# Optimization experiments

Measured on AMD Instinct MI355X. Metric: run time of the kernel, lower is better.

The kernel has to match this reference:

```python
import jax, jax.numpy as jnp
import numpy as np

B, T, D, H, E, O = 4, 2048, 512, 2048, 4, 512
C = 1024  # expert capacity
HE = H // E  # per-expert hidden width


def setup_inputs() -> dict:
    key = jax.random.key(0)
    ks = jax.random.split(key, 7)
    x = jax.random.normal(ks[0], (B, T, D), dtype=jnp.float32)
    dispatch_mask = jax.random.uniform(ks[1], (B, T, E, C), dtype=jnp.float32)
    combine_array = jax.random.uniform(ks[2], (B, T, E, C), dtype=jnp.float32)
    # per-expert parameters (fc1 contract, fc2 expand)
    w1 = jax.random.normal(ks[3], (E, D, HE), dtype=jnp.float32) * (1.0 / np.sqrt(D))
    b1 = jnp.zeros((E, HE), dtype=jnp.float32)
    w2 = jax.random.normal(ks[4], (E, HE, O), dtype=jnp.float32) * (1.0 / np.sqrt(HE))
    b2 = jnp.zeros((O,), dtype=jnp.float32)
    return {"x": x, "dispatch_mask": dispatch_mask, "combine_array": combine_array,
            "w1": w1, "b1": b1, "w2": w2, "b2": b2}


def reference(x, dispatch_mask, combine_array, w1, b1, w2, b2):
    # dispatch: gather tokens into per-expert capacity buffers [B,E,C,D]
    xd = jnp.einsum('btd,btec->becd', x, dispatch_mask)
    # per-expert fc1: [B,E,C,HE]
    h = jnp.einsum('becd,edh->bech', xd, w1) + b1[None, :, None, :]
    # GELU (exact erf form, matching torch nn.GELU default); norm/dropout are identity
    h = jax.nn.gelu(h, approximate=False)
    # per-expert fc2: [B,E,C,O]
    y = jnp.einsum('bech,eho->beco', h, w2)
    # combine: scatter expert outputs back to tokens [B,T,O]
    out = jnp.einsum('beco,btec->bto', y, combine_array) + b2
    return out
```

## Files before the change

### kernel.cpp

```cpp
#include <hip/hip_runtime.h>
#include <math.h>

namespace {

typedef short short8 __attribute__((ext_vector_type(8)));
typedef float f32x4 __attribute__((ext_vector_type(4)));

constexpr int kB = 4, kT = 2048, kD = 512, kE = 4, kC = 1024, kHE = 512,
              kO = 512, kEC = 4096;

__device__ __forceinline__ unsigned short f2bf(float f) {
    unsigned int u = __float_as_uint(f);
    u += 0x7fffu + ((u >> 16) & 1u);
    return (unsigned short)(u >> 16);
}

__device__ __forceinline__ float gelu_exact(float v) {
    return 0.5f * v * (1.0f + erff(v * 0.70710678118654752f));
}

#define GLDS16(g, l)                                                      \
    __builtin_amdgcn_global_load_lds(                                     \
        (const __attribute__((address_space(1))) unsigned int*)(g),       \
        (__attribute__((address_space(3))) unsigned int*)(l), 16, 0, 0)

__global__ __launch_bounds__(256)
void transpose_cast(const float* __restrict__ in, unsigned short* __restrict__ out,
                    int R, int Cc, long long sIn, long long sOut)
{
    __shared__ float tile[32][33];
    const int z = blockIdx.z;
    const float* ip = in + (long long)z * sIn;
    unsigned short* op = out + (long long)z * sOut;
    const int c0 = blockIdx.x * 32, r0 = blockIdx.y * 32;
    const int tx = threadIdx.x & 31, ty = threadIdx.x >> 5;
#pragma unroll
    for (int i = 0; i < 4; ++i) {
        const int r = ty + i * 8;
        tile[r][tx] = ip[(size_t)(r0 + r) * Cc + c0 + tx];
    }
    __syncthreads();
#pragma unroll
    for (int i = 0; i < 4; ++i) {
        const int c = ty + i * 8;
        op[(size_t)(c0 + c) * R + r0 + tx] = f2bf(tile[tx][c]);
    }
}

__global__ __launch_bounds__(256)
void cast_bf16(const float* __restrict__ in, unsigned short* __restrict__ out,
               long long n)
{
    const long long i = ((long long)blockIdx.x * blockDim.x + threadIdx.x) * 4;
    if (i < n) {
        const float4 v = *(const float4*)&in[i];
        unsigned short o[4] = {f2bf(v.x), f2bf(v.y), f2bf(v.z), f2bf(v.w)};
        *(uint2*)&out[i] = *(const uint2*)o;
    }
}

template <int MODE>
__global__ __launch_bounds__(256, 2)
void mfma_gemm(const unsigned short* __restrict__ Aall,
               const unsigned short* __restrict__ Ball,
               const float* __restrict__ biasAll,
               void* __restrict__ Call,
               int M, int N, int K,
               long long sA, long long sB, long long sC,
               int zModA, int zModB, int zModBias, int biasStride, int bShift)
{
    __shared__ unsigned short As[2][128 * 64];
    __shared__ unsigned short Bs[2][128 * 64];

    const int z = blockIdx.z;
    const unsigned short* Ab = Aall + (long long)(z % zModA) * sA;
    const unsigned short* Bb = Ball + (long long)(z % zModB) * sB;
    const float* bias =
        (MODE != 0) ? biasAll + (long long)(z % zModBias) * biasStride : nullptr;

    const int t = threadIdx.x;
    const int lane = t & 63;
    const int w = t >> 6;
    const int wrow = w * 32;
    const int l8r = lane >> 3;
    const int l8c = ((lane & 7) ^ l8r) * 8;
    const int row0 = blockIdx.y * 128;
    const int col0 = blockIdx.x * 128;

    const int wm = (w >> 1) * 64;
    const int wn = (w & 1) * 64;
    const int fr = lane & 15;
    const int fq = (lane >> 4) * 8;
    const int fsw = (fr & 7) * 8;

    const unsigned int bMask = (1u << bShift) - 1u;

    f32x4 acc[4][4] = {};

#define STAGE(buf, k0)                                                        \
    do {                                                                      \
        _Pragma("unroll")                                                     \
        for (int r = 0; r < 4; ++r) {                                         \
            const int ar = row0 + wrow + r * 8 + l8r;                         \
            GLDS16(Ab + (size_t)ar * K + ((k0) + l8c),                        \
                   &As[buf][(wrow + r * 8) * 64]);                            \
            const int bn = col0 + wrow + r * 8 + l8r;                         \
            const int gk = (k0) + l8c;                                        \
            const size_t boff =                                               \
                (((size_t)(gk >> bShift) * N + bn) << bShift) + (gk & bMask); \
            GLDS16(Bb + boff, &Bs[buf][(wrow + r * 8) * 64]);                 \
        }                                                                     \
    } while (0)

    const int nt = K / 64;
    STAGE(0, 0);
    int cur = 0;
    for (int t0 = 0; t0 < nt; ++t0) {
        if (t0 + 1 < nt) {
            STAGE(cur ^ 1, (t0 + 1) * 64);
            asm volatile("s_waitcnt vmcnt(8)" ::: "memory");
        } else {
            asm volatile("s_waitcnt vmcnt(0)" ::: "memory");
        }
        __builtin_amdgcn_s_barrier();
#pragma unroll
        for (int kk = 0; kk < 2; ++kk) {
            short8 af[4], bf[4];
#pragma unroll
            for (int i = 0; i < 4; ++i)
                af[i] = *(const short8*)&As[cur][(wm + i * 16 + fr) * 64 +
                                                 ((kk * 32 + fq) ^ fsw)];
#pragma unroll
            for (int j = 0; j < 4; ++j)
                bf[j] = *(const short8*)&Bs[cur][(wn + j * 16 + fr) * 64 +
                                                 ((kk * 32 + fq) ^ fsw)];
#pragma unroll
            for (int i = 0; i < 4; ++i)
#pragma unroll
                for (int j = 0; j < 4; ++j)
                    acc[i][j] = __builtin_amdgcn_mfma_f32_16x16x32_bf16(
                        af[i], bf[j], acc[i][j], 0, 0, 0);
        }
        asm volatile("s_waitcnt lgkmcnt(0)" ::: "memory");
        __builtin_amdgcn_sched_barrier(0);
        __builtin_amdgcn_s_barrier();
        cur ^= 1;
    }
#undef STAGE

    const long long cz = (long long)z * sC;
#pragma unroll
    for (int i = 0; i < 4; ++i) {
        const int rowb = row0 + wm + i * 16 + (lane >> 4) * 4;
#pragma unroll
        for (int j = 0; j < 4; ++j) {
            const int col = col0 + wn + j * 16 + fr;
            const float bv = (MODE != 0) ? bias[col] : 0.0f;
#pragma unroll
            for (int r = 0; r < 4; ++r) {
                const float v = acc[i][j][r];
                const size_t idx = (size_t)cz + (size_t)(rowb + r) * N + col;
                if (MODE == 0)
                    ((unsigned short*)Call)[idx] = f2bf(v);
                else if (MODE == 1)
                    ((unsigned short*)Call)[idx] = f2bf(gelu_exact(v + bv));
                else
                    ((float*)Call)[idx] = v + bv;
            }
        }
    }
}

}

extern "C" void kernel_launch(void* const* d_in, const int* in_sizes, int n_in,
                              void* d_out, int out_size, void* d_ws, size_t ws_size,
                              hipStream_t stream)
{
    const float* x    = (const float*)d_in[0];
    const float* mask = (const float*)d_in[1];
    const float* comb = (const float*)d_in[2];
    const float* w1   = (const float*)d_in[3];
    const float* b1   = (const float*)d_in[4];
    const float* w2   = (const float*)d_in[5];
    const float* b2   = (const float*)d_in[6];
    float* out = (float*)d_out;

    unsigned short* ws    = (unsigned short*)d_ws;
    unsigned short* regA  = ws;
    unsigned short* xT    = regA + 33554432;
    unsigned short* w1T   = xT + 4194304;
    unsigned short* w2T   = w1T + 1048576;
    unsigned short* xd    = w2T + 1048576;
    unsigned short* h     = xd + 8388608;
    unsigned short* maskT = regA;
    unsigned short* combB = regA;
    unsigned short* yT    = xd;

    dim3 blk(256);

    transpose_cast<<<dim3(kEC / 32, kT / 32, kB), blk, 0, stream>>>(
        mask, maskT, kT, kEC, (long long)kT * kEC, (long long)kT * kEC);
    transpose_cast<<<dim3(kD / 32, kT / 32, kB), blk, 0, stream>>>(
        x, xT, kT, kD, (long long)kT * kD, (long long)kT * kD);
    transpose_cast<<<dim3(kHE / 32, kD / 32, kE), blk, 0, stream>>>(
        w1, w1T, kD, kHE, (long long)kD * kHE, (long long)kD * kHE);
    transpose_cast<<<dim3(kO / 32, kHE / 32, kE), blk, 0, stream>>>(
        w2, w2T, kHE, kO, (long long)kHE * kO, (long long)kHE * kO);

    mfma_gemm<0><<<dim3(kD / 128, kEC / 128, kB), blk, 0, stream>>>(
        maskT, xT, nullptr, xd, kEC, kD, kT,
        (long long)kEC * kT, (long long)kD * kT, (long long)kEC * kD,
        kB, kB, 1, 0, 11);

    cast_bf16<<<dim3(33554432 / 4 / 256), blk, 0, stream>>>(
        comb, combB, 33554432LL);

    mfma_gemm<1><<<dim3(kHE / 128, kC / 128, kB * kE), blk, 0, stream>>>(
        xd, w1T, b1, h, kC, kHE, kD,
        (long long)kC * kD, (long long)kHE * kD, (long long)kC * kHE,
        kB * kE, kE, kE, kHE, 9);

    mfma_gemm<0><<<dim3(kC / 128, kO / 128, kB * kE), blk, 0, stream>>>(
        w2T, h, nullptr, yT, kO, kC, kHE,
        (long long)kO * kHE, (long long)kC * kHE, (long long)kO * kC,
        kE, kB * kE, 1, 0, 9);

    mfma_gemm<3><<<dim3(kO / 128, kT / 128, kB), blk, 0, stream>>>(
        combB, yT, b2, out, kT, kO, kEC,
        (long long)kT * kEC, (long long)kE * kO * kC, (long long)kT * kO,
        kB, kB, 1, 0, 10);
}
```

Measured before the change: 477.2 us.

## Deepen GEMM pipeline to 4 LDS stages with register double-buffered fragments

Changes the bf16 MFMA GEMM from a 2-stage LDS double buffer to a 4-stage ring. LDS fragment reads for the next k-tile are issued with inline ds_read_b128 asm into a second register set while the current set feeds the MFMAs, which removes one barrier per iteration. It also remaps workgroup IDs in groups of 8, likely to improve L2 locality across dies. The cost is double the LDS and more registers, so launch bounds drop to one block per CU-slot and occupancy falls. The loop assumes K/64 is at least 4 and that gridDim.x is a power of two.

New measurement: 442.9 us. 7.2% less time.

```diff
diff --git a/kernel.cpp b/kernel.cpp
--- a/kernel.cpp
+++ b/kernel.cpp
@@ -4,6 +4,7 @@
 namespace {
 
 typedef short short8 __attribute__((ext_vector_type(8)));
+typedef int i32x4 __attribute__((ext_vector_type(4)));
 typedef float f32x4 __attribute__((ext_vector_type(4)));
 
 constexpr int kB = 4, kT = 2048, kD = 512, kE = 4, kC = 1024, kHE = 512,
@@ -60,7 +61,7 @@
 }
 
 template <int MODE>
-__global__ __launch_bounds__(256, 2)
+__global__ __launch_bounds__(256, 1)
 void mfma_gemm(const unsigned short* __restrict__ Aall,
                const unsigned short* __restrict__ Ball,
                const float* __restrict__ biasAll,
@@ -69,14 +70,27 @@
                long long sA, long long sB, long long sC,
                int zModA, int zModB, int zModBias, int biasStride, int bShift)
 {
-    __shared__ unsigned short As[2][128 * 64];
-    __shared__ unsigned short Bs[2][128 * 64];
+    __shared__ unsigned short As[4][128 * 64];
+    __shared__ unsigned short Bs[4][128 * 64];
 
     const int z = blockIdx.z;
     const unsigned short* Ab = Aall + (long long)(z % zModA) * sA;
     const unsigned short* Bb = Ball + (long long)(z % zModB) * sB;
     const float* bias =
         (MODE != 0) ? biasAll + (long long)(z % zModBias) * biasStride : nullptr;
+
+    const int gx = gridDim.x;
+    int lin = blockIdx.y * gx + blockIdx.x;
+    const int nwg = gx * gridDim.y;
+    if ((nwg & 7) == 0) {
+        const int q = nwg >> 3;
+        lin = (lin & 7) * q + (lin >> 3);
+    }
+    const int gxs = 31 - __clz(gx);
+    const int bx = lin & (gx - 1);
+    const int by = lin >> gxs;
+    const int row0 = by * 128;
+    const int colB = bx * 128;
 
     const int t = threadIdx.x;
     const int lane = t & 63;
@@ -84,8 +98,6 @@
     const int wrow = w * 32;
     const int l8r = lane >> 3;
     const int l8c = ((lane & 7) ^ l8r) * 8;
-    const int row0 = blockIdx.y * 128;
-    const int col0 = blockIdx.x * 128;
 
     const int wm = (w >> 1) * 64;
     const int wn = (w & 1) * 64;
@@ -97,6 +109,47 @@
 
     f32x4 acc[4][4] = {};
 
+    const unsigned aB0 =
+        (unsigned)(size_t)(const __attribute__((address_space(3))) unsigned short*)
+            &As[0][0] +
+        (unsigned)(((wm + fr) * 64 + (fq ^ fsw)) * 2);
+    const unsigned bB0 =
+        (unsigned)(size_t)(const __attribute__((address_space(3))) unsigned short*)
+            &Bs[0][0] +
+        (unsigned)(((wn + fr) * 64 + (fq ^ fsw)) * 2);
+
+    struct FragSet { i32x4 a0[4], a1[4], b0[4], b1[4]; };
+    FragSet R0, R1;
+
+#define DSR0(d, a) asm volatile("ds_read_b128 %0, %1" : "=v"(d) : "v"(a))
+#define DSR1(d, a) asm volatile("ds_read_b128 %0, %1 offset:2048" : "=v"(d) : "v"(a))
+#define DSR2(d, a) asm volatile("ds_read_b128 %0, %1 offset:4096" : "=v"(d) : "v"(a))
+#define DSR3(d, a) asm volatile("ds_read_b128 %0, %1 offset:6144" : "=v"(d) : "v"(a))
+
+#define READ16(R, CB)                                                         \
+    do {                                                                      \
+        const unsigned A0c = aB0 + (CB) * 16384u, A1c = A0c ^ 64u;            \
+        const unsigned B0c = bB0 + (CB) * 16384u, B1c = B0c ^ 64u;            \
+        DSR0(R.a0[0], A0c); DSR1(R.a0[1], A0c); DSR2(R.a0[2], A0c); DSR3(R.a0[3], A0c); \
+        DSR0(R.b0[0], B0c); DSR1(R.b0[1], B0c); DSR2(R.b0[2], B0c); DSR3(R.b0[3], B0c); \
+        DSR0(R.a1[0], A1c); DSR1(R.a1[1], A1c); DSR2(R.a1[2], A1c); DSR3(R.a1[3], A1c); \
+        DSR0(R.b1[0], B1c); DSR1(R.b1[1], B1c); DSR2(R.b1[2], B1c); DSR3(R.b1[3], B1c); \
+    } while (0)
+
+#define MFMA16(R)                                                             \
+    do {                                                                      \
+        _Pragma("unroll") for (int i_ = 0; i_ < 4; ++i_)                      \
+            _Pragma("unroll") for (int j_ = 0; j_ < 4; ++j_)                  \
+                acc[i_][j_] = __builtin_amdgcn_mfma_f32_16x16x32_bf16(        \
+                    __builtin_bit_cast(short8, R.a0[i_]),                     \
+                    __builtin_bit_cast(short8, R.b0[j_]), acc[i_][j_], 0, 0, 0); \
+        _Pragma("unroll") for (int i_ = 0; i_ < 4; ++i_)                      \
+            _Pragma("unroll") for (int j_ = 0; j_ < 4; ++j_)                  \
+                acc[i_][j_] = __builtin_amdgcn_mfma_f32_16x16x32_bf16(        \
+                    __builtin_bit_cast(short8, R.a1[i_]),                     \
+                    __builtin_bit_cast(short8, R.b1[j_]), acc[i_][j_], 0, 0, 0); \
+    } while (0)
+
 #define STAGE(buf, k0)                                                        \
     do {                                                                      \
         _Pragma("unroll")                                                     \
@@ -104,7 +157,7 @@
             const int ar = row0 + wrow + r * 8 + l8r;                         \
             GLDS16(Ab + (size_t)ar * K + ((k0) + l8c),                        \
                    &As[buf][(wrow + r * 8) * 64]);                            \
-            const int bn = col0 + wrow + r * 8 + l8r;                         \
+            const int bn = colB + wrow + r * 8 + l8r;                         \
             const int gk = (k0) + l8c;                                        \
             const size_t boff =                                               \
                 (((size_t)(gk >> bShift) * N + bn) << bShift) + (gk & bMask); \
@@ -112,41 +165,51 @@
         }                                                                     \
     } while (0)
 
+#define ITER_FULL(T, CBRD, CBST, Rmf, Rrd)                                    \
+    do {                                                                      \
+        STAGE(CBST, ((T) + 2) * 64);                                          \
+        asm volatile("s_waitcnt vmcnt(8)" ::: "memory");                      \
+        __builtin_amdgcn_s_barrier();                                         \
+        READ16(Rrd, CBRD);                                                    \
+        MFMA16(Rmf);                                                          \
+        asm volatile("s_waitcnt lgkmcnt(0)" ::: "memory");                    \
+        __builtin_amdgcn_sched_barrier(0);                                    \
+    } while (0)
+
     const int nt = K / 64;
+
     STAGE(0, 0);
-    int cur = 0;
-    for (int t0 = 0; t0 < nt; ++t0) {
-        if (t0 + 1 < nt) {
-            STAGE(cur ^ 1, (t0 + 1) * 64);
-            asm volatile("s_waitcnt vmcnt(8)" ::: "memory");
-        } else {
-            asm volatile("s_waitcnt vmcnt(0)" ::: "memory");
-        }
-        __builtin_amdgcn_s_barrier();
-#pragma unroll
-        for (int kk = 0; kk < 2; ++kk) {
-            short8 af[4], bf[4];
-#pragma unroll
-            for (int i = 0; i < 4; ++i)
-                af[i] = *(const short8*)&As[cur][(wm + i * 16 + fr) * 64 +
-                                                 ((kk * 32 + fq) ^ fsw)];
-#pragma unroll
-            for (int j = 0; j < 4; ++j)
-                bf[j] = *(const short8*)&Bs[cur][(wn + j * 16 + fr) * 64 +
-                                                 ((kk * 32 + fq) ^ fsw)];
-#pragma unroll
-            for (int i = 0; i < 4; ++i)
-#pragma unroll
-                for (int j = 0; j < 4; ++j)
-                    acc[i][j] = __builtin_amdgcn_mfma_f32_16x16x32_bf16(
-                        af[i], bf[j], acc[i][j], 0, 0, 0);
-        }
-        asm volatile("s_waitcnt lgkmcnt(0)" ::: "memory");
-        __builtin_amdgcn_sched_barrier(0);
-        __builtin_amdgcn_s_barrier();
-        cur ^= 1;
-    }
+    STAGE(1, 64);
+    asm volatile("s_waitcnt vmcnt(8)" ::: "memory");
+    __builtin_amdgcn_s_barrier();
+    READ16(R0, 0);
+    asm volatile("s_waitcnt lgkmcnt(0)" ::: "memory");
+    __builtin_amdgcn_sched_barrier(0);
+
+    for (int t0 = 0; t0 + 4 < nt; t0 += 4) {
+        ITER_FULL(t0 + 0, 1, 2, R0, R1);
+        ITER_FULL(t0 + 1, 2, 3, R1, R0);
+        ITER_FULL(t0 + 2, 3, 0, R0, R1);
+        ITER_FULL(t0 + 3, 0, 1, R1, R0);
+    }
+    ITER_FULL(nt - 4, 1, 2, R0, R1);
+    ITER_FULL(nt - 3, 2, 3, R1, R0);
+    asm volatile("s_waitcnt vmcnt(0)" ::: "memory");
+    __builtin_amdgcn_s_barrier();
+    READ16(R1, 3);
+    MFMA16(R0);
+    asm volatile("s_waitcnt lgkmcnt(0)" ::: "memory");
+    __builtin_amdgcn_sched_barrier(0);
+    MFMA16(R1);
+
+#undef ITER_FULL
 #undef STAGE
+#undef MFMA16
+#undef READ16
+#undef DSR0
+#undef DSR1
+#undef DSR2
+#undef DSR3
 
     const long long cz = (long long)z * sC;
 #pragma unroll
@@ -154,7 +217,7 @@
         const int rowb = row0 + wm + i * 16 + (lane >> 4) * 4;
 #pragma unroll
         for (int j = 0; j < 4; ++j) {
-            const int col = col0 + wn + j * 16 + fr;
+            const int col = colB + wn + j * 16 + fr;
             const float bv = (MODE != 0) ? bias[col] : 0.0f;
 #pragma unroll
             for (int r = 0; r < 4; ++r) {
```
